# Kernel tuning notes

Measured on AMD Instinct MI355X. Metric: run time of the kernel, lower is better.

The kernel has to match this reference:

```python
import jax, jax.numpy as jnp
import numpy as np
import math

N_EMBD = 1024
N_HEAD = 16
HEAD_DIM = N_EMBD // N_HEAD


def setup_inputs() -> dict:
    key = jax.random.key(0)
    k1, k2, k3 = jax.random.split(key, 3)
    x = jax.random.normal(k1, (2, 2048, N_EMBD), dtype=jnp.float32)
    # nn.Linear(n_embd, 3*n_embd, bias=False): weight shape [3*n_embd, n_embd]
    w_qkv = jax.random.normal(k2, (3 * N_EMBD, N_EMBD), dtype=jnp.float32) * (1.0 / math.sqrt(N_EMBD))
    w_proj = jax.random.normal(k3, (N_EMBD, N_EMBD), dtype=jnp.float32) * (1.0 / math.sqrt(N_EMBD))
    return {"x": x, "w_qkv": w_qkv, "w_proj": w_proj}


def reference(x, w_qkv, w_proj):
    bsz, seq_len, channels = x.shape
    n_head, head_dim = N_HEAD, HEAD_DIM
    # qkv projection: x @ W^T -> [b, s, 3c]
    qkv = jnp.einsum('bsc,dc->bsd', x, w_qkv)
    q, k, v = jnp.split(qkv, 3, axis=2)
    # [b, h, s, hd]
    q = q.reshape(bsz, seq_len, n_head, head_dim).transpose(0, 2, 1, 3)
    k = k.reshape(bsz, seq_len, n_head, head_dim).transpose(0, 2, 1, 3)
    v = v.reshape(bsz, seq_len, n_head, head_dim).transpose(0, 2, 1, 3)
    scale = 1.0 / math.sqrt(head_dim)
    att = jnp.einsum('bhqd,bhkd->bhqk', q, k) * scale  # [b,h,s,s]
    causal = jnp.tril(jnp.ones((seq_len, seq_len), dtype=bool))
    att = jnp.where(causal[None, None, :, :], att, -jnp.inf)
    att = jax.nn.softmax(att, axis=-1)
    # dropout p=0.0 -> identity
    y = jnp.einsum('bhqk,bhkd->bhqd', att, v)
    y = y.transpose(0, 2, 1, 3).reshape(bsz, seq_len, channels)
    return jnp.einsum('bsc,dc->bsd', y, w_proj)
```

## Files before the change

kernel.cpp:

```cpp
#include <hip/hip_runtime.h>
#include <hip/hip_bf16.h>

typedef short short8 __attribute__((ext_vector_type(8)));
typedef float f32x4 __attribute__((ext_vector_type(4)));

#define NB   2
#define SEQ  2048
#define CH   1024
#define NH   16
#define HD   64
#define MROWS (NB*SEQ)
#define QSZ  (NB*NH*SEQ*HD)
#define NX   ((size_t)MROWS * CH)
#define NWQ  ((size_t)3 * CH * CH)
#define NWP  ((size_t)CH * CH)

__device__ __forceinline__ f32x4 mfma16(short8 a, short8 b, f32x4 c) {
    return __builtin_amdgcn_mfma_f32_16x16x32_bf16(a, b, c, 0, 0, 0);
}

__device__ __forceinline__ short bf16_of(float f) {
    return __builtin_bit_cast(short, __float2bfloat16(f));
}

__device__ __forceinline__ short8 load8(const __hip_bfloat16* p) {
    return *reinterpret_cast<const short8*>(p);
}
__device__ __forceinline__ short8 load8(const float* p) {
    f32x4 a = *reinterpret_cast<const f32x4*>(p);
    f32x4 b = *reinterpret_cast<const f32x4*>(p + 4);
    short8 r;
    r[0] = bf16_of(a[0]); r[1] = bf16_of(a[1]);
    r[2] = bf16_of(a[2]); r[3] = bf16_of(a[3]);
    r[4] = bf16_of(b[0]); r[5] = bf16_of(b[1]);
    r[6] = bf16_of(b[2]); r[7] = bf16_of(b[3]);
    return r;
}

__device__ __forceinline__ void gload_lds16(const void* g, void* l) {
    __builtin_amdgcn_global_load_lds(
        (const __attribute__((address_space(1))) unsigned int*)g,
        (__attribute__((address_space(3))) unsigned int*)l, 16, 0, 0);
}

__global__ void cvt3_kernel(const float* __restrict__ x,
                            const float* __restrict__ wq,
                            const float* __restrict__ wp,
                            __hip_bfloat16* __restrict__ dst) {
    const size_t i = ((size_t)blockIdx.x * 256 + threadIdx.x) * 8;
    const float* src;
    size_t off;
    if (i < NX)            { src = x;  off = i; }
    else if (i < NX + NWQ) { src = wq; off = i - NX; }
    else                   { src = wp; off = i - NX - NWQ; }
    *(short8*)&dst[i] = load8(src + off);
}

template<int EPI>
__global__ __launch_bounds__(256, 2)
void gemm_bt2(const __hip_bfloat16* __restrict__ A,
              const __hip_bfloat16* __restrict__ W,
              int K, int N,
              float* __restrict__ Cout,
              __hip_bfloat16* __restrict__ qp,
              __hip_bfloat16* __restrict__ kp,
              __hip_bfloat16* __restrict__ vtp)
{
    __shared__ alignas(16) __hip_bfloat16 Asm[2][128 * 32];
    __shared__ alignas(16) __hip_bfloat16 Bsm[2][128 * 32];

    const int tid  = threadIdx.x;
    const int lane = tid & 63;
    const int wave = tid >> 6;
    const int wm   = wave >> 1, wn = wave & 1;
    const int l15  = lane & 15, lg = lane >> 4;
    const int m0   = blockIdx.x * 128;
    const int n0   = blockIdx.y * 128;

    f32x4 acc[4][4] = {};

    const int srow = lane >> 2;
    const int scol = (lane & 3) * 8;

    auto stage = [&](int buf, int k0) {
        #pragma unroll
        for (int half = 0; half < 2; ++half) {
            const int row = wave * 32 + half * 16;
            gload_lds16(A + (size_t)(m0 + row + srow) * K + k0 + scol,
                        &Asm[buf][row * 32]);
            gload_lds16(W + (size_t)(n0 + row + srow) * K + k0 + scol,
                        &Bsm[buf][row * 32]);
        }
    };

    auto compute = [&](int buf) {
        short8 af[4], bfr[4];
        #pragma unroll
        for (int mi = 0; mi < 4; ++mi)
            af[mi] = *(const short8*)&Asm[buf][(wm * 64 + mi * 16 + l15) * 32 + lg * 8];
        #pragma unroll
        for (int ni = 0; ni < 4; ++ni)
            bfr[ni] = *(const short8*)&Bsm[buf][(wn * 64 + ni * 16 + l15) * 32 + lg * 8];
        #pragma unroll
        for (int mi = 0; mi < 4; ++mi)
            #pragma unroll
            for (int ni = 0; ni < 4; ++ni)
                acc[mi][ni] = mfma16(af[mi], bfr[ni], acc[mi][ni]);
    };

    stage(0, 0);
    int it = 0;
    for (int k0 = 0; k0 < K; k0 += 32, ++it) {
        const int cur = it & 1;
        __syncthreads();
        if (k0 + 32 < K) stage(cur ^ 1, k0 + 32);
        compute(cur);
    }

    #pragma unroll
    for (int mi = 0; mi < 4; ++mi) {
        #pragma unroll
        for (int ni = 0; ni < 4; ++ni) {
            #pragma unroll
            for (int j = 0; j < 4; ++j) {
                const int m = m0 + wm * 64 + mi * 16 + lg * 4 + j;
                const int n = n0 + wn * 64 + ni * 16 + l15;
                if constexpr (EPI == 0) {
                    Cout[(size_t)m * N + n] = acc[mi][ni][j];
                } else {
                    const __hip_bfloat16 hv = __float2bfloat16(acc[mi][ni][j]);
                    const int sec = n >> 10;
                    const int c   = n & 1023;
                    const int h   = c >> 6, d = c & 63;
                    const int b   = m >> 11, s = m & 2047;
                    const int bh  = b * NH + h;
                    if (sec == 0)      qp [((size_t)bh * SEQ + s) * HD + d] = hv;
                    else if (sec == 1) kp [((size_t)bh * SEQ + s) * HD + d] = hv;
                    else               vtp[((size_t)bh * HD  + d) * SEQ + s] = hv;
                }
            }
        }
    }
}

template<int EPI, typename TA, typename TW>
__global__ __launch_bounds__(256, 2)
void gemm_bt(const TA* __restrict__ A,
             const TW* __restrict__ W,
             int K, int N,
             float* __restrict__ Cout,
             __hip_bfloat16* __restrict__ qp,
             __hip_bfloat16* __restrict__ kp,
             __hip_bfloat16* __restrict__ vtp)
{
    __shared__ alignas(16) __hip_bfloat16 Asm[128 * 32];
    __shared__ alignas(16) __hip_bfloat16 Bsm[128 * 32];

    const int tid  = threadIdx.x;
    const int lane = tid & 63;
    const int wave = tid >> 6;
    const int wm   = wave >> 1, wn = wave & 1;
    const int l15  = lane & 15, lg = lane >> 4;
    const int m0   = blockIdx.x * 128;
    const int n0   = blockIdx.y * 128;

    f32x4 acc[4][4] = {};

    const int c0 = tid, c1 = tid + 256;
    const int r0 = c0 >> 2, kc0 = (c0 & 3) << 3;
    const int r1 = c1 >> 2, kc1 = (c1 & 3) << 3;
    const TA* a0p = A + (size_t)(m0 + r0) * K + kc0;
    const TA* a1p = A + (size_t)(m0 + r1) * K + kc1;
    const TW* b0p = W + (size_t)(n0 + r0) * K + kc0;
    const TW* b1p = W + (size_t)(n0 + r1) * K + kc1;

    for (int k0 = 0; k0 < K; k0 += 32) {
        short8 av0 = load8(a0p + k0);
        short8 av1 = load8(a1p + k0);
        short8 bv0 = load8(b0p + k0);
        short8 bv1 = load8(b1p + k0);
        __syncthreads();
        *(short8*)&Asm[c0 * 8] = av0;
        *(short8*)&Asm[c1 * 8] = av1;
        *(short8*)&Bsm[c0 * 8] = bv0;
        *(short8*)&Bsm[c1 * 8] = bv1;
        __syncthreads();

        short8 af[4], bfr[4];
        #pragma unroll
        for (int mi = 0; mi < 4; ++mi)
            af[mi] = *(const short8*)&Asm[(wm * 64 + mi * 16 + l15) * 32 + lg * 8];
        #pragma unroll
        for (int ni = 0; ni < 4; ++ni)
            bfr[ni] = *(const short8*)&Bsm[(wn * 64 + ni * 16 + l15) * 32 + lg * 8];
        #pragma unroll
        for (int mi = 0; mi < 4; ++mi)
            #pragma unroll
            for (int ni = 0; ni < 4; ++ni)
                acc[mi][ni] = mfma16(af[mi], bfr[ni], acc[mi][ni]);
    }

    #pragma unroll
    for (int mi = 0; mi < 4; ++mi) {
        #pragma unroll
        for (int ni = 0; ni < 4; ++ni) {
            #pragma unroll
            for (int j = 0; j < 4; ++j) {
                const int m = m0 + wm * 64 + mi * 16 + lg * 4 + j;
                const int n = n0 + wn * 64 + ni * 16 + l15;
                if constexpr (EPI == 0) {
                    Cout[(size_t)m * N + n] = acc[mi][ni][j];
                } else {
                    const __hip_bfloat16 hv = __float2bfloat16(acc[mi][ni][j]);
                    const int sec = n >> 10;
                    const int c   = n & 1023;
                    const int h   = c >> 6, d = c & 63;
                    const int b   = m >> 11, s = m & 2047;
                    const int bh  = b * NH + h;
                    if (sec == 0)      qp [((size_t)bh * SEQ + s) * HD + d] = hv;
                    else if (sec == 1) kp [((size_t)bh * SEQ + s) * HD + d] = hv;
                    else               vtp[((size_t)bh * HD  + d) * SEQ + s] = hv;
                }
            }
        }
    }
}

__global__ __launch_bounds__(256, 3)
void attn_fwd3(const __hip_bfloat16* __restrict__ qp,
               const __hip_bfloat16* __restrict__ kp,
               const __hip_bfloat16* __restrict__ vtp,
               __hip_bfloat16* __restrict__ yp)
{
    __shared__ alignas(16) __hip_bfloat16 Ksm[2][64 * 64];
    __shared__ alignas(16) __hip_bfloat16 Vsm[2][64 * 64];
    __shared__ alignas(16) __hip_bfloat16 P[4][16][72];

    const int tid  = threadIdx.x;
    const int lane = tid & 63, wave = tid >> 6;
    const int l15  = lane & 15, lg = lane >> 4;
    const int id   = blockIdx.x;
    const int c    = 31 - (id >> 5);
    const int bh   = id & 31;
    const int b    = bh >> 4, h = bh & 15;
    const int q0   = c * 64 + wave * 16;

    const __hip_bfloat16* Q  = qp  + (size_t)bh * SEQ * HD;
    const __hip_bfloat16* Kp = kp  + (size_t)bh * SEQ * HD;
    const __hip_bfloat16* Vt = vtp + (size_t)bh * HD * SEQ;

    short8 qf[2];
    #pragma unroll
    for (int dk = 0; dk < 2; ++dk)
        qf[dk] = *(const short8*)&Q[(size_t)(q0 + l15) * HD + dk * 32 + lg * 8];

    const short ONE = 0x3F80;
    short8 ones;
    #pragma unroll
    for (int i = 0; i < 8; ++i) ones[i] = ONE;

    f32x4 o[4] = {};
    f32x4 accl = {};
    float m_r[4];
    #pragma unroll
    for (int j = 0; j < 4; ++j) m_r[j] = -1e30f;

    auto stage = [&](int buf, int t) {
        const int kv0 = t * 64;
        #pragma unroll
        for (int j = 0; j < 2; ++j) {
            const int ch  = j * 256 + tid;
            const int row = ch >> 3, cb = ch & 7;
            const int cbs = cb ^ (row & 7);
            gload_lds16(Kp + (size_t)(kv0 + row) * HD + cbs * 8,
                        &Ksm[buf][(j * 256 + wave * 64) * 8]);
            gload_lds16(Vt + (size_t)row * SEQ + kv0 + cbs * 8,
                        &Vsm[buf][(j * 256 + wave * 64) * 8]);
        }
    };

    auto compute = [&](int buf, int t) {
        const int kv0 = t * 64;
        f32x4 s[4] = {};
        #pragma unroll
        for (int kf = 0; kf < 4; ++kf)
            #pragma unroll
            for (int dk = 0; dk < 2; ++dk) {
                short8 kfrag = *(const short8*)
                    &Ksm[buf][(kf * 16 + l15) * 64 + (((dk * 4 + lg) ^ (l15 & 7)) * 8)];
                s[kf] = mfma16(qf[dk], kfrag, s[kf]);
            }

        float v[4][4], mx[4];
        const bool diag = (t == c);
        #pragma unroll
        for (int j = 0; j < 4; ++j) {
            const int row = q0 + lg * 4 + j;
            #pragma unroll
            for (int kf = 0; kf < 4; ++kf) {
                float sv = s[kf][j] * 0.125f;
                if (diag && (kv0 + kf * 16 + l15 > row)) sv = -1e30f;
                v[kf][j] = sv;
            }
            mx[j] = fmaxf(fmaxf(v[0][j], v[1][j]), fmaxf(v[2][j], v[3][j]));
        }
        #pragma unroll
        for (int off = 1; off < 16; off <<= 1)
            #pragma unroll
            for (int j = 0; j < 4; ++j)
                mx[j] = fmaxf(mx[j], __shfl_xor(mx[j], off));

        bool needs = false;
        #pragma unroll
        for (int j = 0; j < 4; ++j) needs |= (mx[j] > m_r[j] + 8.0f);
        if (__any(needs)) {
            #pragma unroll
            for (int j = 0; j < 4; ++j) {
                const float mn = fmaxf(m_r[j], mx[j]);
                const float r  = __expf(m_r[j] - mn);
                m_r[j] = mn;
                accl[j] *= r;
                #pragma unroll
                for (int dt = 0; dt < 4; ++dt) o[dt][j] *= r;
            }
        }
        #pragma unroll
        for (int j = 0; j < 4; ++j)
            #pragma unroll
            for (int kf = 0; kf < 4; ++kf)
                v[kf][j] = __expf(v[kf][j] - m_r[j]);

        #pragma unroll
        for (int j = 0; j < 4; ++j)
            #pragma unroll
            for (int kf = 0; kf < 4; ++kf)
                P[wave][lg * 4 + j][kf * 16 + l15] = __float2bfloat16(v[kf][j]);
        asm volatile("s_waitcnt lgkmcnt(0)" ::: "memory");
        __builtin_amdgcn_sched_barrier(0);
        short8 pa0 = *(const short8*)&P[wave][l15][lg * 8];
        short8 pa1 = *(const short8*)&P[wave][l15][32 + lg * 8];

        accl = mfma16(pa0, ones, accl);
        accl = mfma16(pa1, ones, accl);

        #pragma unroll
        for (int dt = 0; dt < 4; ++dt) {
            short8 vf0 = *(const short8*)
                &Vsm[buf][(dt * 16 + l15) * 64 + (((0 + lg) ^ (l15 & 7)) * 8)];
            short8 vf1 = *(const short8*)
                &Vsm[buf][(dt * 16 + l15) * 64 + (((4 + lg) ^ (l15 & 7)) * 8)];
            o[dt] = mfma16(pa0, vf0, o[dt]);
            o[dt] = mfma16(pa1, vf1, o[dt]);
        }
    };

    stage(0, 0);
    for (int t = 0; t <= c; ++t) {
        const int cur = t & 1;
        __syncthreads();
        if (t < c) stage(cur ^ 1, t + 1);
        compute(cur, t);
    }

    #pragma unroll
    for (int j = 0; j < 4; ++j) {
        const float inv_l = 1.0f / accl[j];
        const int s = q0 + lg * 4 + j;
        #pragma unroll
        for (int dt = 0; dt < 4; ++dt) {
            yp[((size_t)(b * SEQ + s)) * CH + h * 64 + dt * 16 + l15] =
                __float2bfloat16(o[dt][j] * inv_l);
        }
    }
}

extern "C" void kernel_launch(void* const* d_in, const int* in_sizes, int n_in,
                              void* d_out, int out_size, void* d_ws, size_t ws_size,
                              hipStream_t stream)
{
    const float* x      = (const float*)d_in[0];
    const float* w_qkv  = (const float*)d_in[1];
    const float* w_proj = (const float*)d_in[2];
    float* out = (float*)d_out;

    __hip_bfloat16* ws = (__hip_bfloat16*)d_ws;

    if (ws_size >= 41943040ull) {
        __hip_bfloat16* xb   = ws;
        __hip_bfloat16* wqb  = ws + NX;
        __hip_bfloat16* wpb  = ws + NX + NWQ;
        __hip_bfloat16* q_ws = ws + NX + NWQ + NWP;
        __hip_bfloat16* k_ws = q_ws + (size_t)QSZ;
        __hip_bfloat16* vt_ws= k_ws + (size_t)QSZ;
        __hip_bfloat16* y_ws = xb;

        cvt3_kernel<<<(NX + NWQ + NWP) / 2048, 256, 0, stream>>>(x, w_qkv, w_proj, ws);

        gemm_bt2<1><<<dim3(MROWS / 128, 3072 / 128), 256, 0, stream>>>(
            xb, wqb, CH, 3 * CH, nullptr, q_ws, k_ws, vt_ws);

        attn_fwd3<<<1024, 256, 0, stream>>>(q_ws, k_ws, vt_ws, y_ws);

        gemm_bt2<0><<<dim3(MROWS / 128, CH / 128), 256, 0, stream>>>(
            y_ws, wpb, CH, CH, out, nullptr, nullptr, nullptr);
    } else {
        __hip_bfloat16* q_ws  = ws;
        __hip_bfloat16* k_ws  = ws + (size_t)QSZ;
        __hip_bfloat16* vt_ws = ws + (size_t)2 * QSZ;
        __hip_bfloat16* y_ws  = ws + (size_t)3 * QSZ;

        gemm_bt<1, float, float><<<dim3(MROWS / 128, 3072 / 128), 256, 0, stream>>>(
            x, w_qkv, CH, 3 * CH, nullptr, q_ws, k_ws, vt_ws);

        attn_fwd3<<<1024, 256, 0, stream>>>(q_ws, k_ws, vt_ws, y_ws);

        gemm_bt<0, __hip_bfloat16, float><<<dim3(MROWS / 128, CH / 128), 256, 0, stream>>>(
            y_ws, w_proj, CH, CH, out, nullptr, nullptr, nullptr);
    }
}
```

Before: 125.7 us.

## Compute transposed S in attention, fold softmax scale into Q, pack P writes

The attention kernel now computes S^T (K as the A operand), so each lane holds one query row. The row max then needs only two cross-lane shuffles instead of sixteen. The 1/sqrt(d) scale moves into the QKV GEMM epilogue, and the probability tile is written to LDS as packed bf16 pairs, halving the number of LDS store instructions. The QKV GEMM launch bound also rises to 3 blocks per CU, which may force register spilling. Rounding Q after scaling by 0.125 is exact, since it is a power of two.

```diff
diff --git a/kernel.cpp b/kernel.cpp
--- a/kernel.cpp
+++ b/kernel.cpp
@@ -21,6 +21,10 @@
 
 __device__ __forceinline__ short bf16_of(float f) {
     return __builtin_bit_cast(short, __float2bfloat16(f));
+}
+__device__ __forceinline__ unsigned int pkbf(float a, float b) {
+    return (unsigned int)(unsigned short)bf16_of(a)
+         | ((unsigned int)(unsigned short)bf16_of(b) << 16);
 }
 
 __device__ __forceinline__ short8 load8(const __hip_bfloat16* p) {
@@ -57,7 +61,7 @@
 }
 
 template<int EPI>
-__global__ __launch_bounds__(256, 2)
+__global__ __launch_bounds__(256, 3)
 void gemm_bt2(const __hip_bfloat16* __restrict__ A,
               const __hip_bfloat16* __restrict__ W,
               int K, int N,
@@ -128,15 +132,21 @@
                 if constexpr (EPI == 0) {
                     Cout[(size_t)m * N + n] = acc[mi][ni][j];
                 } else {
-                    const __hip_bfloat16 hv = __float2bfloat16(acc[mi][ni][j]);
                     const int sec = n >> 10;
                     const int c   = n & 1023;
                     const int h   = c >> 6, d = c & 63;
                     const int b   = m >> 11, s = m & 2047;
                     const int bh  = b * NH + h;
-                    if (sec == 0)      qp [((size_t)bh * SEQ + s) * HD + d] = hv;
-                    else if (sec == 1) kp [((size_t)bh * SEQ + s) * HD + d] = hv;
-                    else               vtp[((size_t)bh * HD  + d) * SEQ + s] = hv;
+                    if (sec == 0) {
+                        qp[((size_t)bh * SEQ + s) * HD + d] =
+                            __float2bfloat16(acc[mi][ni][j] * 0.125f);
+                    } else if (sec == 1) {
+                        kp[((size_t)bh * SEQ + s) * HD + d] =
+                            __float2bfloat16(acc[mi][ni][j]);
+                    } else {
+                        vtp[((size_t)bh * HD + d) * SEQ + s] =
+                            __float2bfloat16(acc[mi][ni][j]);
+                    }
                 }
             }
         }
@@ -211,15 +221,21 @@
                 if constexpr (EPI == 0) {
                     Cout[(size_t)m * N + n] = acc[mi][ni][j];
                 } else {
-                    const __hip_bfloat16 hv = __float2bfloat16(acc[mi][ni][j]);
                     const int sec = n >> 10;
                     const int c   = n & 1023;
                     const int h   = c >> 6, d = c & 63;
                     const int b   = m >> 11, s = m & 2047;
                     const int bh  = b * NH + h;
-                    if (sec == 0)      qp [((size_t)bh * SEQ + s) * HD + d] = hv;
-                    else if (sec == 1) kp [((size_t)bh * SEQ + s) * HD + d] = hv;
-                    else               vtp[((size_t)bh * HD  + d) * SEQ + s] = hv;
+                    if (sec == 0) {
+                        qp[((size_t)bh * SEQ + s) * HD + d] =
+                            __float2bfloat16(acc[mi][ni][j] * 0.125f);
+                    } else if (sec == 1) {
+                        kp[((size_t)bh * SEQ + s) * HD + d] =
+                            __float2bfloat16(acc[mi][ni][j]);
+                    } else {
+                        vtp[((size_t)bh * HD + d) * SEQ + s] =
+                            __float2bfloat16(acc[mi][ni][j]);
+                    }
                 }
             }
         }
@@ -227,14 +243,14 @@
 }
 
 __global__ __launch_bounds__(256, 3)
-void attn_fwd3(const __hip_bfloat16* __restrict__ qp,
+void attn_fwd5(const __hip_bfloat16* __restrict__ qp,
                const __hip_bfloat16* __restrict__ kp,
                const __hip_bfloat16* __restrict__ vtp,
                __hip_bfloat16* __restrict__ yp)
 {
     __shared__ alignas(16) __hip_bfloat16 Ksm[2][64 * 64];
     __shared__ alignas(16) __hip_bfloat16 Vsm[2][64 * 64];
-    __shared__ alignas(16) __hip_bfloat16 P[4][16][72];
+    __shared__ alignas(16) unsigned int Pw[4][16 * 36];
 
     const int tid  = threadIdx.x;
     const int lane = tid & 63, wave = tid >> 6;
@@ -261,9 +277,7 @@
 
     f32x4 o[4] = {};
     f32x4 accl = {};
-    float m_r[4];
-    #pragma unroll
-    for (int j = 0; j < 4; ++j) m_r[j] = -1e30f;
+    float m_r = -1e30f;
 
     auto stage = [&](int buf, int t) {
         const int kv0 = t * 64;
@@ -288,57 +302,62 @@
             for (int dk = 0; dk < 2; ++dk) {
                 short8 kfrag = *(const short8*)
                     &Ksm[buf][(kf * 16 + l15) * 64 + (((dk * 4 + lg) ^ (l15 & 7)) * 8)];
-                s[kf] = mfma16(qf[dk], kfrag, s[kf]);
+                s[kf] = mfma16(kfrag, qf[dk], s[kf]);
             }
 
-        float v[4][4], mx[4];
+        float v[4][4];
         const bool diag = (t == c);
-        #pragma unroll
-        for (int j = 0; j < 4; ++j) {
-            const int row = q0 + lg * 4 + j;
-            #pragma unroll
-            for (int kf = 0; kf < 4; ++kf) {
-                float sv = s[kf][j] * 0.125f;
-                if (diag && (kv0 + kf * 16 + l15 > row)) sv = -1e30f;
+        const int qrow = q0 + l15;
+        #pragma unroll
+        for (int kf = 0; kf < 4; ++kf)
+            #pragma unroll
+            for (int j = 0; j < 4; ++j) {
+                float sv = s[kf][j];
+                if (diag && (kv0 + kf * 16 + lg * 4 + j > qrow)) sv = -1e30f;
                 v[kf][j] = sv;
             }
-            mx[j] = fmaxf(fmaxf(v[0][j], v[1][j]), fmaxf(v[2][j], v[3][j]));
-        }
-        #pragma unroll
-        for (int off = 1; off < 16; off <<= 1)
+        float mxv = v[0][0];
+        #pragma unroll
+        for (int kf = 0; kf < 4; ++kf)
             #pragma unroll
             for (int j = 0; j < 4; ++j)
-                mx[j] = fmaxf(mx[j], __shfl_xor(mx[j], off));
-
-        bool needs = false;
-        #pragma unroll
-        for (int j = 0; j < 4; ++j) needs |= (mx[j] > m_r[j] + 8.0f);
-        if (__any(needs)) {
+                mxv = fmaxf(mxv, v[kf][j]);
+        mxv = fmaxf(mxv, __shfl_xor(mxv, 16));
+        mxv = fmaxf(mxv, __shfl_xor(mxv, 32));
+
+        if (__any(mxv > m_r + 8.0f)) {
+            const float mn = fmaxf(m_r, mxv);
+            const float r  = __expf(m_r - mn);
+            m_r = mn;
+            float rj[4];
+            #pragma unroll
+            for (int j = 0; j < 4; ++j)
+                rj[j] = __shfl(r, lg * 4 + j);
             #pragma unroll
             for (int j = 0; j < 4; ++j) {
-                const float mn = fmaxf(m_r[j], mx[j]);
-                const float r  = __expf(m_r[j] - mn);
-                m_r[j] = mn;
-                accl[j] *= r;
+                accl[j] *= rj[j];
                 #pragma unroll
-                for (int dt = 0; dt < 4; ++dt) o[dt][j] *= r;
+                for (int dt = 0; dt < 4; ++dt) o[dt][j] *= rj[j];
             }
         }
-        #pragma unroll
-        for (int j = 0; j < 4; ++j)
-            #pragma unroll
-            for (int kf = 0; kf < 4; ++kf)
-                v[kf][j] = __expf(v[kf][j] - m_r[j]);
-
-        #pragma unroll
-        for (int j = 0; j < 4; ++j)
-            #pragma unroll
-            for (int kf = 0; kf < 4; ++kf)
-                P[wave][lg * 4 + j][kf * 16 + l15] = __float2bfloat16(v[kf][j]);
+
+        #pragma unroll
+        for (int kf = 0; kf < 4; ++kf)
+            #pragma unroll
+            for (int j = 0; j < 4; ++j)
+                v[kf][j] = __expf(v[kf][j] - m_r);
+
+        unsigned int* myP = &Pw[wave][0];
+        const int pb = l15 * 36 + lg * 2;
+        #pragma unroll
+        for (int kf = 0; kf < 4; ++kf) {
+            myP[pb + kf * 8]     = pkbf(v[kf][0], v[kf][1]);
+            myP[pb + kf * 8 + 1] = pkbf(v[kf][2], v[kf][3]);
+        }
         asm volatile("s_waitcnt lgkmcnt(0)" ::: "memory");
         __builtin_amdgcn_sched_barrier(0);
-        short8 pa0 = *(const short8*)&P[wave][l15][lg * 8];
-        short8 pa1 = *(const short8*)&P[wave][l15][32 + lg * 8];
+        short8 pa0 = *(const short8*)&Pw[wave][l15 * 36 + lg * 4];
+        short8 pa1 = *(const short8*)&Pw[wave][l15 * 36 + 16 + lg * 4];
 
         accl = mfma16(pa0, ones, accl);
         accl = mfma16(pa1, ones, accl);
@@ -399,7 +418,7 @@
         gemm_bt2<1><<<dim3(MROWS / 128, 3072 / 128), 256, 0, stream>>>(
             xb, wqb, CH, 3 * CH, nullptr, q_ws, k_ws, vt_ws);
 
-        attn_fwd3<<<1024, 256, 0, stream>>>(q_ws, k_ws, vt_ws, y_ws);
+        attn_fwd5<<<1024, 256, 0, stream>>>(q_ws, k_ws, vt_ws, y_ws);
 
         gemm_bt2<0><<<dim3(MROWS / 128, CH / 128), 256, 0, stream>>>(
             y_ws, wpb, CH, CH, out, nullptr, nullptr, nullptr);
@@ -412,7 +431,7 @@
         gemm_bt<1, float, float><<<dim3(MROWS / 128, 3072 / 128), 256, 0, stream>>>(
             x, w_qkv, CH, 3 * CH, nullptr, q_ws, k_ws, vt_ws);
 
-        attn_fwd3<<<1024, 256, 0, stream>>>(q_ws, k_ws, vt_ws, y_ws);
+        attn_fwd5<<<1024, 256, 0, stream>>>(q_ws, k_ws, vt_ws, y_ws);
 
         gemm_bt<0, __hip_bfloat16, float><<<dim3(MROWS / 128, CH / 128), 256, 0, stream>>>(
             y_ws, w_proj, CH, CH, out, nullptr, nullptr, nullptr);
```

New measurement: 115.2 us. -8.3%, faster.
